# Optimization experiments

Hardware: AMD Instinct MI355X
Metric: run time of the kernel (lower is better)

Reference implementation:

```python
import jax, jax.numpy as jnp
import numpy as np

N_NODES = 100000
N_EDGES = 1200000
NODE_IN = 64
EDGE_IN = 32
HIDDEN = 64


def _glorot(key, shape):
    fan_in, fan_out = shape[0], shape[1]
    s = jnp.sqrt(2.0 / (fan_in + fan_out))
    return jax.random.normal(key, shape, dtype=jnp.float32) * s


def setup_inputs() -> dict:
    key = jax.random.key(0)
    ks = jax.random.split(key, 16)
    inp = {
        "x": jax.random.normal(ks[0], (N_NODES, NODE_IN), dtype=jnp.float32),
        "edge_index": jax.random.randint(ks[1], (2, N_EDGES), 0, N_NODES, dtype=jnp.int64),
        "edge_attr": jax.random.normal(ks[2], (N_EDGES, EDGE_IN), dtype=jnp.float32),
        # SAGE layer 0 (in=NODE_IN -> HIDDEN): lin_l (neighbors, has bias), lin_r (root)
        "w_l0": _glorot(ks[3], (NODE_IN, HIDDEN)),
        "w_r0": _glorot(ks[4], (NODE_IN, HIDDEN)),
        "b0": jnp.zeros((HIDDEN,), jnp.float32),
        "ln_g0": jnp.ones((HIDDEN,), jnp.float32),
        "ln_b0": jnp.zeros((HIDDEN,), jnp.float32),
        # SAGE layer 1 (HIDDEN -> HIDDEN)
        "w_l1": _glorot(ks[5], (HIDDEN, HIDDEN)),
        "w_r1": _glorot(ks[6], (HIDDEN, HIDDEN)),
        "b1": jnp.zeros((HIDDEN,), jnp.float32),
        "ln_g1": jnp.ones((HIDDEN,), jnp.float32),
        "ln_b1": jnp.zeros((HIDDEN,), jnp.float32),
        # Edge classifier MLP: in_dim = 3*HIDDEN + EDGE_IN = 224
        "cw1": _glorot(ks[7], (3 * HIDDEN + EDGE_IN, HIDDEN)),
        "cb1": jnp.zeros((HIDDEN,), jnp.float32),
        "cw2": _glorot(ks[8], (HIDDEN, HIDDEN // 2)),
        "cb2": jnp.zeros((HIDDEN // 2,), jnp.float32),
        "cw3": _glorot(ks[9], (HIDDEN // 2, 1)),
        "cb3": jnp.zeros((1,), jnp.float32),
    }
    return inp


def _sage_conv(x, src, dst, w_l, w_r, b):
    # mean-aggregate source features at destination nodes (PyG SAGEConv, aggr='mean')
    n = x.shape[0]
    msg = x[src]  # [E, F] gather
    agg = jax.ops.segment_sum(msg, dst, num_segments=n)
    cnt = jax.ops.segment_sum(jnp.ones((src.shape[0], 1), x.dtype), dst, num_segments=n)
    mean = agg / jnp.maximum(cnt, 1.0)
    return mean @ w_l + x @ w_r + b


def _layer_norm(x, g, b, eps=1e-5):
    mu = jnp.mean(x, axis=-1, keepdims=True)
    var = jnp.var(x, axis=-1, keepdims=True)
    return (x - mu) * jax.lax.rsqrt(var + eps) * g + b


def reference(x, edge_index, edge_attr,
              w_l0, w_r0, b0, ln_g0, ln_b0,
              w_l1, w_r1, b1, ln_g1, ln_b1,
              cw1, cb1, cw2, cb2, cw3, cb3):
    src, dst = edge_index[0], edge_index[1]
    # Encoder (eval mode: dropout is identity)
    h = jax.nn.relu(_layer_norm(_sage_conv(x, src, dst, w_l0, w_r0, b0), ln_g0, ln_b0))
    z = jax.nn.relu(_layer_norm(_sage_conv(h, src, dst, w_l1, w_r1, b1), ln_g1, ln_b1))
    # Edge classifier: gather-concat-MLP
    z_src = z[src]
    z_dst = z[dst]
    edge_repr = jnp.concatenate([z_src, z_dst, z_src * z_dst, edge_attr], axis=-1)
    h1 = jax.nn.relu(edge_repr @ cw1 + cb1)
    h2 = jax.nn.relu(h1 @ cw2 + cb2)
    logits = (h2 @ cw3 + cb3).squeeze(-1)  # [E]
    return logits
```

## Files before the change

### kernel.cpp

```cpp
#include <hip/hip_runtime.h>
#include <hip/hip_bf16.h>

#define N_NODES 100000
#define N_EDGES 1200000

typedef __attribute__((ext_vector_type(8))) short bfrag;
typedef __attribute__((ext_vector_type(4))) float ffrag;
typedef __attribute__((ext_vector_type(4))) float nf4;

union FragU { uint4 v; uint32_t u[4]; bfrag f; };

__device__ __forceinline__ ushort bfbits(float a) {
  union { __hip_bfloat16 h; ushort u; } c; c.h = __float2bfloat16(a); return c.u;
}
__device__ __forceinline__ uint32_t pkbf(float a, float b) {
  union { __hip_bfloat162 h; uint32_t u; } c;
  c.h = __float22bfloat162_rn(float2{a, b}); return c.u;
}
__device__ __forceinline__ uint32_t mul2bf(uint32_t a, uint32_t b) {
  union { uint32_t u; __hip_bfloat162 h; } x, y, r;
  x.u = a; y.u = b; r.h = __hmul2(x.h, y.h); return r.u;
}
__device__ __forceinline__ float bflo(uint32_t u) { return __int_as_float(u << 16); }
__device__ __forceinline__ float bfhi(uint32_t u) { return __int_as_float(u & 0xffff0000u); }

template <int CTRL>
__device__ __forceinline__ float dpp_add16(float v) {
  int x = __builtin_amdgcn_update_dpp(0, __float_as_int(v), CTRL, 0xF, 0xF, true);
  return v + __int_as_float(x);
}
__device__ __forceinline__ float reduce16(float v) {
  v = dpp_add16<0xB1>(v);
  v = dpp_add16<0x4E>(v);
  v = dpp_add16<0x141>(v);
  v = dpp_add16<0x140>(v);
  return v;
}


__global__ void cvt_k(const float* __restrict__ x, ushort* __restrict__ xb, int n2) {
  int i = blockIdx.x * blockDim.x + threadIdx.x;
  if (i < n2) {
    float a = __builtin_nontemporal_load(x + i * 2);
    float b = __builtin_nontemporal_load(x + i * 2 + 1);
    ((uint32_t*)xb)[i] = pkbf(a, b);
  }
}


__global__ void hist_k(const int* __restrict__ ei, int* __restrict__ deg,
                       int* __restrict__ rank, int E) {
  int e = blockIdx.x * blockDim.x + threadIdx.x;
  if (e < E) rank[e] = atomicAdd(&deg[ei[E + e]], 1);
}

__global__ __launch_bounds__(1024) void scan1_k(const int* __restrict__ deg,
                                                int* __restrict__ off,
                                                int* __restrict__ bsum, int n) {
  __shared__ int wpart[16];
  __shared__ int wpre[16];
  int tid = threadIdx.x, lane = tid & 63, wid = tid >> 6;
  int i = blockIdx.x * 1024 + tid;
  int v = (i < n) ? deg[i] : 0;
  int x = v;
  #pragma unroll
  for (int o = 1; o < 64; o <<= 1) {
    int y = __shfl_up(x, o);
    if (lane >= o) x += y;
  }
  if (lane == 63) wpart[wid] = x;
  __syncthreads();
  if (tid == 0) {
    int run = 0;
    #pragma unroll
    for (int w = 0; w < 16; w++) { int t = wpart[w]; wpre[w] = run; run += t; }
    bsum[blockIdx.x] = run;
  }
  __syncthreads();
  if (i < n) off[i] = x - v + wpre[wid];
}

__global__ void scan2_k(const int* __restrict__ bsum, int* __restrict__ bpre,
                        int* __restrict__ off, int nb, int n) {
  if (threadIdx.x == 0) {
    int run = 0;
    for (int b = 0; b < nb; b++) { int t = bsum[b]; bpre[b] = run; run += t; }
    off[n] = run;
  }
}

__global__ __launch_bounds__(1024) void scan3_k(int* __restrict__ off,
                                                const int* __restrict__ bpre, int n) {
  int i = blockIdx.x * 1024 + threadIdx.x;
  if (i < n) off[i] += bpre[blockIdx.x];
}

__global__ void fill_k(const int* __restrict__ ei, const int* __restrict__ off,
                       const int* __restrict__ rank, int* __restrict__ csr, int E) {
  int e = blockIdx.x * blockDim.x + threadIdx.x;
  if (e < E) {
    int d = ei[E + e];
    int p = off[d] + rank[e];
    __builtin_nontemporal_store(ei[e], &csr[p]);
  }
}


__global__ __launch_bounds__(256) void agg_k(
    const ushort* __restrict__ Xb, const int* __restrict__ off, const int* __restrict__ csr,
    ushort* __restrict__ aggout, int n) {
  int lane = threadIdx.x & 63;
  int quad = lane >> 4, f8 = lane & 15;
  int wave = blockIdx.x * 4 + (threadIdx.x >> 6);
  int nw = gridDim.x * 4;
  int nquads = (n + 3) >> 2;
  const uint2* X2 = (const uint2*)Xb;
  for (int p = wave; p < nquads; p += nw) {
    int i = p * 4 + quad;
    int ic = i < n ? i : n - 1;
    int s0 = off[ic], s1 = off[ic + 1];
    float a0 = 0.f, a1 = 0.f, a2 = 0.f, a3 = 0.f;
    for (int j = s0; j < s1; j += 8) {
      int id[8]; uint2 us[8];
      #pragma unroll
      for (int u = 0; u < 8; u++) {
        int jj = j + u;
        id[u] = __builtin_nontemporal_load(csr + (jj < s1 ? jj : s1 - 1));
      }
      #pragma unroll
      for (int u = 0; u < 8; u++) us[u] = X2[(size_t)id[u] * 16 + f8];
      #pragma unroll
      for (int u = 0; u < 8; u++) {
        if (j + u < s1) {
          a0 += bflo(us[u].x); a1 += bfhi(us[u].x);
          a2 += bflo(us[u].y); a3 += bfhi(us[u].y);
        }
      }
    }
    if (i < n) {
      float rdeg = 1.f / fmaxf((float)(s1 - s0), 1.f);
      uint2 w;
      w.x = pkbf(a0 * rdeg, a1 * rdeg);
      w.y = pkbf(a2 * rdeg, a3 * rdeg);
      ((uint2*)aggout)[(size_t)i * 16 + f8] = w;
    }
  }
}


__global__ __launch_bounds__(256) void node_k(
    const ushort* __restrict__ agg, const ushort* __restrict__ selfb,
    const float* __restrict__ wl, const float* __restrict__ wr,
    const float* __restrict__ bias, const float* __restrict__ g, const float* __restrict__ lb,
    ushort* __restrict__ outb, int n) {
  __shared__ ushort wt[64 * 128];
  const int tid = threadIdx.x;
  for (int i = tid; i < 8192; i += 256) {
    int k = i >> 6, nn = i & 63;
    float v = (k < 64) ? wl[k * 64 + nn] : wr[(k - 64) * 64 + nn];
    wt[nn * 128 + (((k >> 3) ^ (nn & 7)) * 8) + (k & 7)] = bfbits(v);
  }
  __syncthreads();
  const int lane = tid & 63, wid = tid >> 6;
  const int ln = lane & 15, q = lane >> 4;
  float bias_n[4], g_n[4], lb_n[4];
  #pragma unroll
  for (int nt = 0; nt < 4; nt++) {
    bias_n[nt] = bias[nt * 16 + ln];
    g_n[nt] = g[nt * 16 + ln];
    lb_n[nt] = lb[nt * 16 + ln];
  }
  const int ntiles = (n + 15) >> 4;
  for (int t = blockIdx.x * 4 + wid; t < ntiles; t += gridDim.x * 4) {
    int node = t * 16 + ln;
    int nc = node < n ? node : n - 1;
    FragU afr[4];
    #pragma unroll
    for (int kk = 0; kk < 2; kk++) {
      afr[kk].v     = ((const uint4*)agg)[(size_t)nc * 8 + kk * 4 + q];
      afr[2 + kk].v = ((const uint4*)selfb)[(size_t)nc * 8 + kk * 4 + q];
    }
    ffrag acc[4];
    #pragma unroll
    for (int nt = 0; nt < 4; nt++) acc[nt] = ffrag{0.f, 0.f, 0.f, 0.f};
    #pragma unroll
    for (int kk = 0; kk < 4; kk++) {
      bfrag a = afr[kk].f;
      #pragma unroll
      for (int nt = 0; nt < 4; nt++) {
        int nn = nt * 16 + ln;
        int b = kk * 4 + q;
        const bfrag* bp = (const bfrag*)&wt[nn * 128 + ((b ^ (nn & 7)) * 8)];
        acc[nt] = __builtin_amdgcn_mfma_f32_16x16x32_bf16(a, *bp, acc[nt], 0, 0, 0);
      }
    }
    #pragma unroll
    for (int r = 0; r < 4; r++) {
      int m = t * 16 + q * 4 + r;
      float o[4];
      #pragma unroll
      for (int nt = 0; nt < 4; nt++) o[nt] = acc[nt][r] + bias_n[nt];
      float s = (o[0] + o[1]) + (o[2] + o[3]);
      #pragma unroll
      for (int mm = 1; mm < 16; mm <<= 1) s += __shfl_xor(s, mm);
      float mu = s * (1.f / 64.f);
      float v2 = 0.f;
      #pragma unroll
      for (int nt = 0; nt < 4; nt++) { float d2 = o[nt] - mu; v2 += d2 * d2; }
      #pragma unroll
      for (int mm = 1; mm < 16; mm <<= 1) v2 += __shfl_xor(v2, mm);
      float rs = rsqrtf(v2 * (1.f / 64.f) + 1e-5f);
      if (m < n) {
        #pragma unroll
        for (int nt = 0; nt < 4; nt++) {
          float y = fmaxf((o[nt] - mu) * rs * g_n[nt] + lb_n[nt], 0.f);
          outb[(size_t)m * 64 + nt * 16 + ln] = bfbits(y);
        }
      }
    }
  }
}


__global__ __launch_bounds__(256, 2) void edge_mfma_k(
    const int* __restrict__ ei, const float* __restrict__ ea,
    const ushort* __restrict__ zb,
    const float* __restrict__ cw1, const float* __restrict__ cb1,
    const float* __restrict__ cw2, const float* __restrict__ cb2,
    const float* __restrict__ cw3, const float* __restrict__ cb3,
    float* __restrict__ out, int E) {
  __shared__ ushort smem[64 * 256];
  __shared__ ushort ws2[2048];
  const int tid = threadIdx.x;

  for (int i = tid; i < 224 * 64; i += 256) {
    int k = i >> 6, n = i & 63;
    int blk = k >> 3;
    smem[n * 256 + ((blk ^ (n & 7)) * 8) + (k & 7)] = bfbits(cw1[i]);
  }
  __syncthreads();

  const int lane = tid & 63, wid = tid >> 6;
  const int ln = lane & 15, q = lane >> 4;

  FragU w1f[7][4];
  #pragma unroll
  for (int kk = 0; kk < 7; kk++) {
    #pragma unroll
    for (int tt = 0; tt < 4; tt++) {
      int n = tt * 16 + ln;
      int b = kk * 4 + q;
      w1f[kk][tt].v = *(const uint4*)&smem[n * 256 + ((b ^ (n & 7)) * 8)];
    }
  }
  if (wid == 0) {
    #pragma unroll
    for (int t2 = 0; t2 < 2; t2++) {
      #pragma unroll
      for (int kk = 0; kk < 2; kk++) {
        uint32_t w[4];
        #pragma unroll
        for (int p = 0; p < 4; p++) {
          int k = kk * 32 + q * 8 + p * 2;
          int n = t2 * 16 + ln;
          w[p] = pkbf(cw2[k * 32 + n], cw2[(k + 1) * 32 + n]);
        }
        *(uint4*)&ws2[((t2 * 2 + kk) * 64 + lane) * 8] = make_uint4(w[0], w[1], w[2], w[3]);
      }
    }
  }
  __syncthreads();
  ushort* hb = &smem[wid * 1024];

  float cb1v[4];
  #pragma unroll
  for (int t = 0; t < 4; t++) cb1v[t] = cb1[t * 16 + ln];
  float cb2a = cb2[ln], cb2b = cb2[16 + ln];
  float w3a = cw3[ln], w3b = cw3[16 + ln];
  float cb3v = cb3[0];

  const int nt = E >> 4;
  const int S = gridDim.x * 4;
  const int S3 = 3 * S;
  const int w0 = blockIdx.x * 4 + wid;
  const uint4* Z4 = (const uint4*)zb;
  const nf4* EA4 = (const nf4*)ea;

  FragU zA[4], zB[4], zC[4];
  int svA, dvA, svB, dvB, svC, dvC;

  auto prol = [&](FragU (&z)[4], int &sv, int &dv, int u) {
    int uc = u < nt ? u : nt - 1;
    int e = uc * 16 + ln;
    int s = __builtin_nontemporal_load(ei + e);
    int d = __builtin_nontemporal_load(ei + E + e);
    z[0].v = Z4[(size_t)s * 8 + q];
    z[1].v = Z4[(size_t)s * 8 + 4 + q];
    z[2].v = Z4[(size_t)d * 8 + q];
    z[3].v = Z4[(size_t)d * 8 + 4 + q];
    int un = u + S3 < nt ? u + S3 : nt - 1;
    sv = __builtin_nontemporal_load(ei + un * 16 + ln);
    dv = __builtin_nontemporal_load(ei + E + un * 16 + ln);
  };
  prol(zA, svA, dvA, w0);
  prol(zB, svB, dvB, w0 + S);
  prol(zC, svC, dvC, w0 + 2 * S);

  auto half = [&](FragU (&z)[4], int &sv, int &dv, int u) {
    int uc = u < nt ? u : nt - 1;
    int e = uc * 16 + ln;
    nf4 l0 = __builtin_nontemporal_load(EA4 + (size_t)e * 8 + q * 2);
    nf4 l1 = __builtin_nontemporal_load(EA4 + (size_t)e * 8 + q * 2 + 1);

    ffrag acc1[4];
    #pragma unroll
    for (int tt = 0; tt < 4; tt++) acc1[tt] = ffrag{0.f, 0.f, 0.f, 0.f};
    #pragma unroll
    for (int kk = 0; kk < 7; kk++) {
      FragU af;
      if (kk < 4) af = z[kk];
      else if (kk < 6) {
        #pragma unroll
        for (int p = 0; p < 4; p++) af.u[p] = mul2bf(z[kk - 4].u[p], z[kk - 2].u[p]);
      } else {
        af.u[0] = pkbf(l0.x, l0.y); af.u[1] = pkbf(l0.z, l0.w);
        af.u[2] = pkbf(l1.x, l1.y); af.u[3] = pkbf(l1.z, l1.w);
      }
      bfrag a = af.f;
      #pragma unroll
      for (int tt = 0; tt < 4; tt++)
        acc1[tt] = __builtin_amdgcn_mfma_f32_16x16x32_bf16(a, w1f[kk][tt].f, acc1[tt], 0, 0, 0);
    }

    {
      z[0].v = Z4[(size_t)sv * 8 + q];
      z[1].v = Z4[(size_t)sv * 8 + 4 + q];
      z[2].v = Z4[(size_t)dv * 8 + q];
      z[3].v = Z4[(size_t)dv * 8 + 4 + q];
      int uf = u + 2 * S3 < nt ? u + 2 * S3 : nt - 1;
      sv = __builtin_nontemporal_load(ei + uf * 16 + ln);
      dv = __builtin_nontemporal_load(ei + E + uf * 16 + ln);
    }

    #pragma unroll
    for (int tt = 0; tt < 4; tt++) {
      #pragma unroll
      for (int r = 0; r < 4; r++) {
        int m = q * 4 + r;
        int col = tt * 16 + ln;
        float v = fmaxf(acc1[tt][r] + cb1v[tt], 0.f);
        hb[m * 64 + (((col >> 3) ^ (m & 7)) * 8) + (col & 7)] = bfbits(v);
      }
    }

    ffrag acc2[2];
    acc2[0] = ffrag{0.f, 0.f, 0.f, 0.f};
    acc2[1] = ffrag{0.f, 0.f, 0.f, 0.f};
    #pragma unroll
    for (int kk = 0; kk < 2; kk++) {
      int b = kk * 4 + q;
      const bfrag* ap = (const bfrag*)&hb[ln * 64 + ((b ^ (ln & 7)) * 8)];
      bfrag a2 = *ap;
      const bfrag* b0p = (const bfrag*)&ws2[((0 * 2 + kk) * 64 + lane) * 8];
      const bfrag* b1p = (const bfrag*)&ws2[((1 * 2 + kk) * 64 + lane) * 8];
      acc2[0] = __builtin_amdgcn_mfma_f32_16x16x32_bf16(a2, *b0p, acc2[0], 0, 0, 0);
      acc2[1] = __builtin_amdgcn_mfma_f32_16x16x32_bf16(a2, *b1p, acc2[1], 0, 0, 0);
    }

    float p0 = fmaxf(acc2[0][0] + cb2a, 0.f) * w3a + fmaxf(acc2[1][0] + cb2b, 0.f) * w3b;
    float p1 = fmaxf(acc2[0][1] + cb2a, 0.f) * w3a + fmaxf(acc2[1][1] + cb2b, 0.f) * w3b;
    float p2 = fmaxf(acc2[0][2] + cb2a, 0.f) * w3a + fmaxf(acc2[1][2] + cb2b, 0.f) * w3b;
    float p3 = fmaxf(acc2[0][3] + cb2a, 0.f) * w3a + fmaxf(acc2[1][3] + cb2b, 0.f) * w3b;
    p0 = reduce16(p0); p1 = reduce16(p1); p2 = reduce16(p2); p3 = reduce16(p3);
    float keep = (ln == 0) ? p0 : (ln == 1) ? p1 : (ln == 2) ? p2 : p3;
    if (u < nt && ln < 4)
      __builtin_nontemporal_store(keep + cb3v, &out[u * 16 + q * 4 + ln]);
  };

  for (int t = w0; t < nt; t += S3) {
    half(zA, svA, dvA, t);
    half(zB, svB, dvB, t + S);
    half(zC, svC, dvC, t + 2 * S);
  }
}


extern "C" void kernel_launch(void* const* d_in, const int* in_sizes, int n_in,
                              void* d_out, int out_size, void* d_ws, size_t ws_size,
                              hipStream_t stream) {
  const float* x   = (const float*)d_in[0];
  const int*   ei  = (const int*)d_in[1];
  const float* ea  = (const float*)d_in[2];
  const float* wl0 = (const float*)d_in[3];
  const float* wr0 = (const float*)d_in[4];
  const float* b0  = (const float*)d_in[5];
  const float* g0  = (const float*)d_in[6];
  const float* lb0 = (const float*)d_in[7];
  const float* wl1 = (const float*)d_in[8];
  const float* wr1 = (const float*)d_in[9];
  const float* b1  = (const float*)d_in[10];
  const float* g1  = (const float*)d_in[11];
  const float* lb1 = (const float*)d_in[12];
  const float* cw1 = (const float*)d_in[13];
  const float* cb1 = (const float*)d_in[14];
  const float* cw2 = (const float*)d_in[15];
  const float* cb2 = (const float*)d_in[16];
  const float* cw3 = (const float*)d_in[17];
  const float* cb3 = (const float*)d_in[18];
  float* out = (float*)d_out;
  const int N = N_NODES, E = N_EDGES;
  const int NB = (N + 1023) / 1024;

  uintptr_t pp = (uintptr_t)d_ws;
  auto alloc = [&](size_t bytes) {
    uintptr_t r = (pp + 255) & ~(uintptr_t)255; pp = r + bytes; return (void*)r;
  };
  int* deg  = (int*)alloc((size_t)N * 4);
  int* off  = (int*)alloc((size_t)(N + 1) * 4);
  int* rank = (int*)alloc((size_t)E * 4);
  int* csr  = (int*)alloc((size_t)E * 4);
  int* bsum = (int*)alloc((size_t)NB * 4);
  int* bpre = (int*)alloc((size_t)NB * 4);
  ushort* xb  = (ushort*)alloc((size_t)N * 64 * 2);
  ushort* agg = (ushort*)alloc((size_t)N * 64 * 2);
  ushort* hb  = (ushort*)alloc((size_t)N * 64 * 2);
  ushort* zb  = (ushort*)alloc((size_t)N * 64 * 2);

  hipMemsetAsync(deg, 0, (size_t)N * 4, stream);
  cvt_k<<<(N * 32 + 255) / 256, 256, 0, stream>>>(x, xb, N * 32);
  hist_k<<<(E + 255) / 256, 256, 0, stream>>>(ei, deg, rank, E);
  scan1_k<<<NB, 1024, 0, stream>>>(deg, off, bsum, N);
  scan2_k<<<1, 64, 0, stream>>>(bsum, bpre, off, NB, N);
  scan3_k<<<NB, 1024, 0, stream>>>(off, bpre, N);
  fill_k<<<(E + 255) / 256, 256, 0, stream>>>(ei, off, rank, csr, E);
  agg_k<<<2048, 256, 0, stream>>>(xb, off, csr, agg, N);
  node_k<<<512, 256, 0, stream>>>(agg, xb, wl0, wr0, b0, g0, lb0, hb, N);
  agg_k<<<2048, 256, 0, stream>>>(hb, off, csr, agg, N);
  node_k<<<512, 256, 0, stream>>>(agg, hb, wl1, wr1, b1, g1, lb1, zb, N);
  edge_mfma_k<<<512, 256, 0, stream>>>(ei, ea, zb, cw1, cb1, cw2, cb2, cw3, cb3, out, E);
}
```

Measured before the change: 503.4 us.

## Prefetch node tiles, widen aggregation unroll, use DPP reductions and vector loads

node_k now double-buffers its A-fragment loads so the next tiles are fetched while the current tile's MFMA and LayerNorm run, and its grid doubles to 1024 blocks. The mean-aggregation kernel unrolls 16 neighbours per batch instead of 8 and drops nontemporal hints on CSR index loads. LayerNorm row reductions switch from shfl_xor to the existing DPP reduce16 helper, and the bf16 conversion kernel uses one 8-byte vector load. These aim to hide gather latency and cut shuffle overhead, at the cost of more registers and possible occupancy loss, plus wasted loads on degree-padded tails.

```diff
diff --git a/kernel.cpp b/kernel.cpp
--- a/kernel.cpp
+++ b/kernel.cpp
@@ -7,6 +7,7 @@
 typedef __attribute__((ext_vector_type(8))) short bfrag;
 typedef __attribute__((ext_vector_type(4))) float ffrag;
 typedef __attribute__((ext_vector_type(4))) float nf4;
+typedef __attribute__((ext_vector_type(2))) float nf2;
 
 union FragU { uint4 v; uint32_t u[4]; bfrag f; };
 
@@ -41,9 +42,8 @@
 __global__ void cvt_k(const float* __restrict__ x, ushort* __restrict__ xb, int n2) {
   int i = blockIdx.x * blockDim.x + threadIdx.x;
   if (i < n2) {
-    float a = __builtin_nontemporal_load(x + i * 2);
-    float b = __builtin_nontemporal_load(x + i * 2 + 1);
-    ((uint32_t*)xb)[i] = pkbf(a, b);
+    nf2 v = __builtin_nontemporal_load(((const nf2*)x) + i);
+    ((uint32_t*)xb)[i] = pkbf(v.x, v.y);
   }
 }
 
@@ -120,17 +120,17 @@
     int ic = i < n ? i : n - 1;
     int s0 = off[ic], s1 = off[ic + 1];
     float a0 = 0.f, a1 = 0.f, a2 = 0.f, a3 = 0.f;
-    for (int j = s0; j < s1; j += 8) {
-      int id[8]; uint2 us[8];
-      #pragma unroll
-      for (int u = 0; u < 8; u++) {
+    for (int j = s0; j < s1; j += 16) {
+      int id[16]; uint2 us[16];
+      #pragma unroll
+      for (int u = 0; u < 16; u++) {
         int jj = j + u;
-        id[u] = __builtin_nontemporal_load(csr + (jj < s1 ? jj : s1 - 1));
-      }
-      #pragma unroll
-      for (int u = 0; u < 8; u++) us[u] = X2[(size_t)id[u] * 16 + f8];
-      #pragma unroll
-      for (int u = 0; u < 8; u++) {
+        id[u] = csr[jj < s1 ? jj : s1 - 1];
+      }
+      #pragma unroll
+      for (int u = 0; u < 16; u++) us[u] = X2[(size_t)id[u] * 16 + f8];
+      #pragma unroll
+      for (int u = 0; u < 16; u++) {
         if (j + u < s1) {
           a0 += bflo(us[u].x); a1 += bfhi(us[u].x);
           a2 += bflo(us[u].y); a3 += bfhi(us[u].y);
@@ -171,15 +171,21 @@
     lb_n[nt] = lb[nt * 16 + ln];
   }
   const int ntiles = (n + 15) >> 4;
-  for (int t = blockIdx.x * 4 + wid; t < ntiles; t += gridDim.x * 4) {
-    int node = t * 16 + ln;
+  const int S = gridDim.x * 4;
+  int t0 = blockIdx.x * 4 + wid;
+
+  auto loadfrag = [&](FragU (&afr)[4], int t) {
+    int tc = t < ntiles ? t : ntiles - 1;
+    int node = tc * 16 + ln;
     int nc = node < n ? node : n - 1;
-    FragU afr[4];
     #pragma unroll
     for (int kk = 0; kk < 2; kk++) {
       afr[kk].v     = ((const uint4*)agg)[(size_t)nc * 8 + kk * 4 + q];
       afr[2 + kk].v = ((const uint4*)selfb)[(size_t)nc * 8 + kk * 4 + q];
     }
+  };
+
+  auto compute = [&](FragU (&afr)[4], int t) {
     ffrag acc[4];
     #pragma unroll
     for (int nt = 0; nt < 4; nt++) acc[nt] = ffrag{0.f, 0.f, 0.f, 0.f};
@@ -201,14 +207,12 @@
       #pragma unroll
       for (int nt = 0; nt < 4; nt++) o[nt] = acc[nt][r] + bias_n[nt];
       float s = (o[0] + o[1]) + (o[2] + o[3]);
-      #pragma unroll
-      for (int mm = 1; mm < 16; mm <<= 1) s += __shfl_xor(s, mm);
+      s = reduce16(s);
       float mu = s * (1.f / 64.f);
       float v2 = 0.f;
       #pragma unroll
       for (int nt = 0; nt < 4; nt++) { float d2 = o[nt] - mu; v2 += d2 * d2; }
-      #pragma unroll
-      for (int mm = 1; mm < 16; mm <<= 1) v2 += __shfl_xor(v2, mm);
+      v2 = reduce16(v2);
       float rs = rsqrtf(v2 * (1.f / 64.f) + 1e-5f);
       if (m < n) {
         #pragma unroll
@@ -218,6 +222,17 @@
         }
       }
     }
+  };
+
+  if (t0 >= ntiles) return;
+  FragU fA[4], fB[4];
+  loadfrag(fA, t0);
+  loadfrag(fB, t0 + S);
+  for (int t = t0; t < ntiles; t += 2 * S) {
+    compute(fA, t);
+    loadfrag(fA, t + 2 * S);
+    if (t + S < ntiles) compute(fB, t + S);
+    loadfrag(fB, t + 3 * S);
   }
 }
 
@@ -434,8 +449,8 @@
   scan3_k<<<NB, 1024, 0, stream>>>(off, bpre, N);
   fill_k<<<(E + 255) / 256, 256, 0, stream>>>(ei, off, rank, csr, E);
   agg_k<<<2048, 256, 0, stream>>>(xb, off, csr, agg, N);
-  node_k<<<512, 256, 0, stream>>>(agg, xb, wl0, wr0, b0, g0, lb0, hb, N);
+  node_k<<<1024, 256, 0, stream>>>(agg, xb, wl0, wr0, b0, g0, lb0, hb, N);
   agg_k<<<2048, 256, 0, stream>>>(hb, off, csr, agg, N);
-  node_k<<<512, 256, 0, stream>>>(agg, hb, wl1, wr1, b1, g1, lb1, zb, N);
+  node_k<<<1024, 256, 0, stream>>>(agg, hb, wl1, wr1, b1, g1, lb1, zb, N);
   edge_mfma_k<<<512, 256, 0, stream>>>(ei, ea, zb, cw1, cb1, cw2, cb2, cw3, cb3, out, E);
 }
```

Measured after the change: 503.4 us. Within noise of the previous version (-0.0%).
